# Optimization experiments

Hardware: AMD Instinct MI355X
Metric: run time of the kernel (lower is better)

Reference implementation:

```python
import jax, jax.numpy as jnp
import numpy as np

B, T, H = 32, 4096, 1024

def setup_inputs() -> dict:
    key = jax.random.key(0)
    k1, k2 = jax.random.split(key)
    decoder_state = jax.random.normal(k1, (B, H), dtype=jnp.float32)
    encoder_hiddens = jax.random.normal(k2, (B, T, H), dtype=jnp.float32)
    return {"decoder_state": decoder_state, "encoder_hiddens": encoder_hiddens}

def reference(decoder_state, encoder_hiddens):
    # Faithful to the original: torch.sum(s_t * h_t) reduces over batch AND
    # hidden, so score[:, t] is one scalar broadcast to every batch row.
    # scores: [T]
    scores = jnp.einsum('bh,bth->t', decoder_state, encoder_hiddens)
    batch_size = encoder_hiddens.shape[0]
    attention_score = jnp.broadcast_to(scores[None, :], (batch_size, scores.shape[0]))
    attention_distribution = jax.nn.softmax(attention_score, axis=1)  # [B, T]
    # context_vector[b] = sum_t dist[b, t] * encoder_hiddens[b, t]
    context_vector = jnp.einsum('bt,bth->bh', attention_distribution, encoder_hiddens)
    return context_vector
```

## Files before the change

kernel.cpp:

```cpp
#include <hip/hip_runtime.h>
#include <math.h>

#define B_ 32
#define T_ 4096
#define H_ 1024
#define H4_ 256
#define NCHUNK_ 64
#define TPC_ 64

__global__ __launch_bounds__(256) void scores_kernel(
    const float4* __restrict__ s4, const float4* __restrict__ eh4,
    float* __restrict__ scores)
{
    const int t   = blockIdx.x;
    const int tid = threadIdx.x;

    float acc = 0.f;
#pragma unroll 8
    for (int k = 0; k < 32; ++k) {
        int idx4 = tid + k * 256;
        int b    = idx4 >> 8;
        int h4   = idx4 & 255;
        float4 e  = eh4[((size_t)b * T_ + t) * H4_ + h4];
        float4 sv = s4[idx4];
        acc += e.x * sv.x + e.y * sv.y + e.z * sv.z + e.w * sv.w;
    }

    for (int off = 32; off > 0; off >>= 1)
        acc += __shfl_down(acc, off, 64);
    __shared__ float red[4];
    if ((tid & 63) == 0) red[tid >> 6] = acc;
    __syncthreads();
    if (tid == 0) scores[t] = red[0] + red[1] + red[2] + red[3];
}

__global__ __launch_bounds__(256) void softmax_kernel(
    const float* __restrict__ scores, float* __restrict__ dist)
{
    const int tid = threadIdx.x;
    __shared__ float redm[4];
    __shared__ float reds[4];

    float v[16];
    float m = -INFINITY;
#pragma unroll
    for (int k = 0; k < 16; ++k) {
        v[k] = scores[tid + k * 256];
        m = fmaxf(m, v[k]);
    }
    for (int off = 32; off > 0; off >>= 1)
        m = fmaxf(m, __shfl_down(m, off, 64));
    if ((tid & 63) == 0) redm[tid >> 6] = m;
    __syncthreads();
    const float M = fmaxf(fmaxf(redm[0], redm[1]), fmaxf(redm[2], redm[3]));

    float e[16];
    float sum = 0.f;
#pragma unroll
    for (int k = 0; k < 16; ++k) {
        e[k] = expf(v[k] - M);
        sum += e[k];
    }
    for (int off = 32; off > 0; off >>= 1)
        sum += __shfl_down(sum, off, 64);
    if ((tid & 63) == 0) reds[tid >> 6] = sum;
    __syncthreads();
    const float L = reds[0] + reds[1] + reds[2] + reds[3];
    const float inv = 1.f / L;
#pragma unroll
    for (int k = 0; k < 16; ++k)
        dist[tid + k * 256] = e[k] * inv;
}

__global__ __launch_bounds__(256) void context_kernel(
    const float4* __restrict__ eh4, const float* __restrict__ dist,
    float4* __restrict__ part4)
{
    const int chunk = blockIdx.x;
    const int b     = blockIdx.y;
    const int tid   = threadIdx.x;

    const float4* base = eh4 + ((size_t)b * T_ + (size_t)chunk * TPC_) * H4_ + tid;
    const float*  wbase = dist + chunk * TPC_;

    float4 acc = make_float4(0.f, 0.f, 0.f, 0.f);
#pragma unroll 8
    for (int i = 0; i < TPC_; ++i) {
        float  w = wbase[i];
        float4 e = base[(size_t)i * H4_];
        acc.x += w * e.x;
        acc.y += w * e.y;
        acc.z += w * e.z;
        acc.w += w * e.w;
    }
    part4[((size_t)chunk * B_ + b) * H4_ + tid] = acc;
}

__global__ __launch_bounds__(256) void reduce_kernel(
    const float4* __restrict__ part4, float4* __restrict__ out4)
{
    const int o4 = blockIdx.x * 256 + threadIdx.x;
    float4 acc = make_float4(0.f, 0.f, 0.f, 0.f);
#pragma unroll 8
    for (int c = 0; c < NCHUNK_; ++c) {
        float4 p = part4[(size_t)c * (B_ * H4_) + o4];
        acc.x += p.x;
        acc.y += p.y;
        acc.z += p.z;
        acc.w += p.w;
    }
    out4[o4] = acc;
}

extern "C" void kernel_launch(void* const* d_in, const int* in_sizes, int n_in,
                              void* d_out, int out_size, void* d_ws, size_t ws_size,
                              hipStream_t stream) {
    const float* s  = (const float*)d_in[0];
    const float* eh = (const float*)d_in[1];

    float* ws     = (float*)d_ws;
    float* scores = ws;
    float* dist   = ws + T_;
    float4* part4 = (float4*)(ws + 2 * T_);

    scores_kernel<<<T_, 256, 0, stream>>>((const float4*)s, (const float4*)eh, scores);
    softmax_kernel<<<1, 256, 0, stream>>>(scores, dist);
    context_kernel<<<dim3(NCHUNK_, B_), 256, 0, stream>>>((const float4*)eh, dist, part4);
    reduce_kernel<<<(B_ * H4_) / 256, 256, 0, stream>>>(part4, (float4*)d_out);
}
```

Measured before the change: 775.7 us.

## Restructure score pass into per-batch chunk tiles and reverse context chunk order

```diff
diff --git a/kernel.cpp b/kernel.cpp
--- a/kernel.cpp
+++ b/kernel.cpp
@@ -8,34 +8,47 @@
 #define NCHUNK_ 64
 #define TPC_ 64
 
-__global__ __launch_bounds__(256) void scores_kernel(
+__global__ __launch_bounds__(256) void pscores_kernel(
     const float4* __restrict__ s4, const float4* __restrict__ eh4,
-    float* __restrict__ scores)
+    float* __restrict__ pscores)
 {
-    const int t   = blockIdx.x;
-    const int tid = threadIdx.x;
+    const int chunk = blockIdx.x;
+    const int b     = blockIdx.y;
+    const int tid   = threadIdx.x;
+    const int lane  = tid & 63;
+    const int w     = tid >> 6;
 
-    float acc = 0.f;
-#pragma unroll 8
-    for (int k = 0; k < 32; ++k) {
-        int idx4 = tid + k * 256;
-        int b    = idx4 >> 8;
-        int h4   = idx4 & 255;
-        float4 e  = eh4[((size_t)b * T_ + t) * H4_ + h4];
-        float4 sv = s4[idx4];
-        acc += e.x * sv.x + e.y * sv.y + e.z * sv.z + e.w * sv.w;
+    __shared__ float4 sS[H4_];
+    sS[tid] = s4[b * H4_ + tid];
+    __syncthreads();
+    const float4 s0 = sS[lane];
+    const float4 s1 = sS[lane + 64];
+    const float4 s2 = sS[lane + 128];
+    const float4 s3 = sS[lane + 192];
+
+    const float4* ehb = eh4 + ((size_t)b * T_ + (size_t)chunk * TPC_) * H4_;
+
+#pragma unroll 4
+    for (int i = 0; i < TPC_ / 4; ++i) {
+        const int tl = w + 4 * i;
+        const float4* row = ehb + (size_t)tl * H4_;
+        float4 e0 = row[lane];
+        float4 e1 = row[lane + 64];
+        float4 e2 = row[lane + 128];
+        float4 e3 = row[lane + 192];
+        float d = e0.x * s0.x + e0.y * s0.y + e0.z * s0.z + e0.w * s0.w
+                + e1.x * s1.x + e1.y * s1.y + e1.z * s1.z + e1.w * s1.w
+                + e2.x * s2.x + e2.y * s2.y + e2.z * s2.z + e2.w * s2.w
+                + e3.x * s3.x + e3.y * s3.y + e3.z * s3.z + e3.w * s3.w;
+        for (int off = 32; off > 0; off >>= 1)
+            d += __shfl_down(d, off, 64);
+        if (lane == 0)
+            pscores[(chunk * TPC_ + tl) * B_ + b] = d;
     }
-
-    for (int off = 32; off > 0; off >>= 1)
-        acc += __shfl_down(acc, off, 64);
-    __shared__ float red[4];
-    if ((tid & 63) == 0) red[tid >> 6] = acc;
-    __syncthreads();
-    if (tid == 0) scores[t] = red[0] + red[1] + red[2] + red[3];
 }
 
 __global__ __launch_bounds__(256) void softmax_kernel(
-    const float* __restrict__ scores, float* __restrict__ dist)
+    const float4* __restrict__ ps4, float* __restrict__ dist)
 {
     const int tid = threadIdx.x;
     __shared__ float redm[4];
@@ -45,8 +58,16 @@
     float m = -INFINITY;
 #pragma unroll
     for (int k = 0; k < 16; ++k) {
-        v[k] = scores[tid + k * 256];
-        m = fmaxf(m, v[k]);
+        const int t = tid + k * 256;
+        const float4* p = ps4 + (size_t)t * (B_ / 4);
+        float s = 0.f;
+#pragma unroll
+        for (int j = 0; j < B_ / 4; ++j) {
+            float4 q = p[j];
+            s += q.x + q.y + q.z + q.w;
+        }
+        v[k] = s;
+        m = fmaxf(m, s);
     }
     for (int off = 32; off > 0; off >>= 1)
         m = fmaxf(m, __shfl_down(m, off, 64));
@@ -76,11 +97,11 @@
     const float4* __restrict__ eh4, const float* __restrict__ dist,
     float4* __restrict__ part4)
 {
-    const int chunk = blockIdx.x;
+    const int chunk = (NCHUNK_ - 1) - blockIdx.x;
     const int b     = blockIdx.y;
     const int tid   = threadIdx.x;
 
-    const float4* base = eh4 + ((size_t)b * T_ + (size_t)chunk * TPC_) * H4_ + tid;
+    const float4* base  = eh4 + ((size_t)b * T_ + (size_t)chunk * TPC_) * H4_ + tid;
     const float*  wbase = dist + chunk * TPC_;
 
     float4 acc = make_float4(0.f, 0.f, 0.f, 0.f);
@@ -118,13 +139,15 @@
     const float* s  = (const float*)d_in[0];
     const float* eh = (const float*)d_in[1];
 
-    float* ws     = (float*)d_ws;
-    float* scores = ws;
-    float* dist   = ws + T_;
-    float4* part4 = (float4*)(ws + 2 * T_);
+    float* ws      = (float*)d_ws;
+    float* pscores = ws;
+    float* dist    = ws + (size_t)T_ * B_;
+    float4* part4  = (float4*)(dist + T_);
 
-    scores_kernel<<<T_, 256, 0, stream>>>((const float4*)s, (const float4*)eh, scores);
-    softmax_kernel<<<1, 256, 0, stream>>>(scores, dist);
-    context_kernel<<<dim3(NCHUNK_, B_), 256, 0, stream>>>((const float4*)eh, dist, part4);
+    pscores_kernel<<<dim3(NCHUNK_, B_), 256, 0, stream>>>(
+        (const float4*)s, (const float4*)eh, pscores);
+    softmax_kernel<<<1, 256, 0, stream>>>((const float4*)pscores, dist);
+    context_kernel<<<dim3(NCHUNK_, B_), 256, 0, stream>>>(
+        (const float4*)eh, dist, part4);
     reduce_kernel<<<(B_ * H4_) / 256, 256, 0, stream>>>(part4, (float4*)d_out);
 }
```

Measured after the change: 802.3 us. +3.4%, slower.

## Fuse scores, softmax and context into single-pass online-softmax kernel

Applied to the files above, without the earlier changes.

```diff
diff --git a/kernel.cpp b/kernel.cpp
--- a/kernel.cpp
+++ b/kernel.cpp
@@ -1,113 +1,131 @@
 #include <hip/hip_runtime.h>
 #include <math.h>
 
-#define B_ 32
-#define T_ 4096
-#define H_ 1024
+#define B_  32
+#define T_  4096
+#define H_  1024
 #define H4_ 256
-#define NCHUNK_ 64
-#define TPC_ 64
+#define G_  256
+#define TPG_ (T_ / G_)
+#define BH4_ (B_ * H4_)
 
-__global__ __launch_bounds__(256) void scores_kernel(
+__global__ __launch_bounds__(1024) void flash_kernel(
     const float4* __restrict__ s4, const float4* __restrict__ eh4,
-    float* __restrict__ scores)
+    float4* __restrict__ Og4, float* __restrict__ mg, float* __restrict__ lg)
 {
-    const int t   = blockIdx.x;
-    const int tid = threadIdx.x;
+    const int g    = blockIdx.x;
+    const int tid  = threadIdx.x;
+    const int lane = tid & 63;
+    const int w    = tid >> 6;
+    const int b    = tid >> 5;
+    const int hb   = tid & 31;
 
-    float acc = 0.f;
-#pragma unroll 8
-    for (int k = 0; k < 32; ++k) {
-        int idx4 = tid + k * 256;
-        int b    = idx4 >> 8;
-        int h4   = idx4 & 255;
-        float4 e  = eh4[((size_t)b * T_ + t) * H4_ + h4];
-        float4 sv = s4[idx4];
-        acc += e.x * sv.x + e.y * sv.y + e.z * sv.z + e.w * sv.w;
+    __shared__ float redw[16];
+    __shared__ float sc_sh;
+
+    float4 sreg[8];
+#pragma unroll
+    for (int j = 0; j < 8; ++j)
+        sreg[j] = s4[b * H4_ + hb + 32 * j];
+
+    const float4* ep = eh4 + ((size_t)b * T_ + (size_t)g * TPG_) * H4_ + hb;
+
+    float4 acc[8];
+#pragma unroll
+    for (int j = 0; j < 8; ++j) acc[j] = make_float4(0.f, 0.f, 0.f, 0.f);
+    float m = -INFINITY, l = 0.f;
+
+    for (int i = 0; i < TPG_; ++i) {
+        float4 e[8];
+#pragma unroll
+        for (int j = 0; j < 8; ++j) e[j] = ep[32 * j];
+        ep += H4_;
+
+        float p = 0.f;
+#pragma unroll
+        for (int j = 0; j < 8; ++j)
+            p += e[j].x * sreg[j].x + e[j].y * sreg[j].y
+               + e[j].z * sreg[j].z + e[j].w * sreg[j].w;
+
+        for (int off = 32; off > 0; off >>= 1)
+            p += __shfl_down(p, off, 64);
+        if (lane == 0) redw[w] = p;
+        __syncthreads();
+        if (w == 0) {
+            float q = (lane < 16) ? redw[lane] : 0.f;
+            q += __shfl_down(q, 8, 64);
+            q += __shfl_down(q, 4, 64);
+            q += __shfl_down(q, 2, 64);
+            q += __shfl_down(q, 1, 64);
+            if (lane == 0) sc_sh = q;
+        }
+        __syncthreads();
+        const float score = sc_sh;
+
+        const float mn    = fmaxf(m, score);
+        const float alpha = __expf(m - mn);
+        const float wgt   = __expf(score - mn);
+        l = l * alpha + wgt;
+#pragma unroll
+        for (int j = 0; j < 8; ++j) {
+            acc[j].x = acc[j].x * alpha + wgt * e[j].x;
+            acc[j].y = acc[j].y * alpha + wgt * e[j].y;
+            acc[j].z = acc[j].z * alpha + wgt * e[j].z;
+            acc[j].w = acc[j].w * alpha + wgt * e[j].w;
+        }
+        m = mn;
     }
 
-    for (int off = 32; off > 0; off >>= 1)
-        acc += __shfl_down(acc, off, 64);
-    __shared__ float red[4];
-    if ((tid & 63) == 0) red[tid >> 6] = acc;
-    __syncthreads();
-    if (tid == 0) scores[t] = red[0] + red[1] + red[2] + red[3];
+    float4* op = Og4 + (size_t)g * BH4_ + b * H4_ + hb;
+#pragma unroll
+    for (int j = 0; j < 8; ++j) op[32 * j] = acc[j];
+    if (tid == 0) { mg[g] = m; lg[g] = l; }
 }
 
-__global__ __launch_bounds__(256) void softmax_kernel(
-    const float* __restrict__ scores, float* __restrict__ dist)
+__global__ __launch_bounds__(64) void combine_kernel(
+    const float4* __restrict__ Og4, const float* __restrict__ mg,
+    const float* __restrict__ lg, float4* __restrict__ out4)
 {
     const int tid = threadIdx.x;
-    __shared__ float redm[4];
-    __shared__ float reds[4];
+    __shared__ float wsh[G_];
 
-    float v[16];
-    float m = -INFINITY;
+    float mv[4];
+    float M = -INFINITY;
 #pragma unroll
-    for (int k = 0; k < 16; ++k) {
-        v[k] = scores[tid + k * 256];
-        m = fmaxf(m, v[k]);
+    for (int j = 0; j < 4; ++j) {
+        mv[j] = mg[tid + 64 * j];
+        M = fmaxf(M, mv[j]);
     }
     for (int off = 32; off > 0; off >>= 1)
-        m = fmaxf(m, __shfl_down(m, off, 64));
-    if ((tid & 63) == 0) redm[tid >> 6] = m;
+        M = fmaxf(M, __shfl_down(M, off, 64));
+    M = __shfl(M, 0, 64);
+
+    float Ls = 0.f;
+#pragma unroll
+    for (int j = 0; j < 4; ++j)
+        Ls += lg[tid + 64 * j] * __expf(mv[j] - M);
+    for (int off = 32; off > 0; off >>= 1)
+        Ls += __shfl_down(Ls, off, 64);
+    Ls = __shfl(Ls, 0, 64);
+    const float invL = 1.f / Ls;
+
+#pragma unroll
+    for (int j = 0; j < 4; ++j)
+        wsh[tid + 64 * j] = __expf(mv[j] - M) * invL;
     __syncthreads();
-    const float M = fmaxf(fmaxf(redm[0], redm[1]), fmaxf(redm[2], redm[3]));
 
-    float e[16];
-    float sum = 0.f;
-#pragma unroll
-    for (int k = 0; k < 16; ++k) {
-        e[k] = expf(v[k] - M);
-        sum += e[k];
-    }
-    for (int off = 32; off > 0; off >>= 1)
-        sum += __shfl_down(sum, off, 64);
-    if ((tid & 63) == 0) reds[tid >> 6] = sum;
-    __syncthreads();
-    const float L = reds[0] + reds[1] + reds[2] + reds[3];
-    const float inv = 1.f / L;
-#pragma unroll
-    for (int k = 0; k < 16; ++k)
-        dist[tid + k * 256] = e[k] * inv;
-}
-
-__global__ __launch_bounds__(256) void context_kernel(
-    const float4* __restrict__ eh4, const float* __restrict__ dist,
-    float4* __restrict__ part4)
-{
-    const int chunk = blockIdx.x;
-    const int b     = blockIdx.y;
-    const int tid   = threadIdx.x;
-
-    const float4* base = eh4 + ((size_t)b * T_ + (size_t)chunk * TPC_) * H4_ + tid;
-    const float*  wbase = dist + chunk * TPC_;
-
+    const int o4 = blockIdx.x * 64 + tid;
     float4 acc = make_float4(0.f, 0.f, 0.f, 0.f);
-#pragma unroll 8
-    for (int i = 0; i < TPC_; ++i) {
-        float  w = wbase[i];
-        float4 e = base[(size_t)i * H4_];
-        acc.x += w * e.x;
-        acc.y += w * e.y;
-        acc.z += w * e.z;
-        acc.w += w * e.w;
-    }
-    part4[((size_t)chunk * B_ + b) * H4_ + tid] = acc;
-}
-
-__global__ __launch_bounds__(256) void reduce_kernel(
-    const float4* __restrict__ part4, float4* __restrict__ out4)
-{
-    const int o4 = blockIdx.x * 256 + threadIdx.x;
-    float4 acc = make_float4(0.f, 0.f, 0.f, 0.f);
-#pragma unroll 8
-    for (int c = 0; c < NCHUNK_; ++c) {
-        float4 p = part4[(size_t)c * (B_ * H4_) + o4];
-        acc.x += p.x;
-        acc.y += p.y;
-        acc.z += p.z;
-        acc.w += p.w;
+    for (int gg = 0; gg < G_; gg += 4) {
+        float4 a0 = Og4[(size_t)(gg + 0) * BH4_ + o4];
+        float4 a1 = Og4[(size_t)(gg + 1) * BH4_ + o4];
+        float4 a2 = Og4[(size_t)(gg + 2) * BH4_ + o4];
+        float4 a3 = Og4[(size_t)(gg + 3) * BH4_ + o4];
+        float w0 = wsh[gg], w1 = wsh[gg + 1], w2 = wsh[gg + 2], w3 = wsh[gg + 3];
+        acc.x += w0 * a0.x + w1 * a1.x + w2 * a2.x + w3 * a3.x;
+        acc.y += w0 * a0.y + w1 * a1.y + w2 * a2.y + w3 * a3.y;
+        acc.z += w0 * a0.z + w1 * a1.z + w2 * a2.z + w3 * a3.z;
+        acc.w += w0 * a0.w + w1 * a1.w + w2 * a2.w + w3 * a3.w;
     }
     out4[o4] = acc;
 }
@@ -118,13 +136,12 @@
     const float* s  = (const float*)d_in[0];
     const float* eh = (const float*)d_in[1];
 
-    float* ws     = (float*)d_ws;
-    float* scores = ws;
-    float* dist   = ws + T_;
-    float4* part4 = (float4*)(ws + 2 * T_);
+    float4* Og4 = (float4*)d_ws;
+    float*  mg  = (float*)(Og4 + (size_t)G_ * BH4_);
+    float*  lg  = mg + G_;
 
-    scores_kernel<<<T_, 256, 0, stream>>>((const float4*)s, (const float4*)eh, scores);
-    softmax_kernel<<<1, 256, 0, stream>>>(scores, dist);
-    context_kernel<<<dim3(NCHUNK_, B_), 256, 0, stream>>>((const float4*)eh, dist, part4);
-    reduce_kernel<<<(B_ * H4_) / 256, 256, 0, stream>>>(part4, (float4*)d_out);
+    flash_kernel<<<G_, 1024, 0, stream>>>(
+        (const float4*)s, (const float4*)eh, Og4, mg, lg);
+    combine_kernel<<<BH4_ / 64, 64, 0, stream>>>(
+        Og4, mg, lg, (float4*)d_out);
 }
```

After: 700.2 us. -9.7%, faster.
